# Performance work log

Measured on AMD Instinct MI355X. Metric: run time of the kernel, lower is better.

## Reference

```python
import jax, jax.numpy as jnp
import numpy as np

N = 50000   # nodes
E = 800000  # edges
D = 128     # input_dim
H = 128     # hidden_dim
C = 40      # output_dim (classes)


def setup_inputs() -> dict:
    key = jax.random.key(0)
    ks = jax.random.split(key, 8)
    x = jax.random.normal(ks[0], (N, D), dtype=jnp.float32)
    edge_index = jax.random.randint(ks[1], (2, E), 0, N, dtype=jnp.int32)
    sD = 1.0 / np.sqrt(D)
    sH = 1.0 / np.sqrt(H)
    W1 = jax.random.uniform(ks[2], (D, H), jnp.float32, -sD, sD)
    b1 = jnp.zeros((H,), jnp.float32)
    W2 = jax.random.uniform(ks[3], (H, H), jnp.float32, -sH, sH)
    b2 = jnp.zeros((H,), jnp.float32)
    W3 = jax.random.uniform(ks[4], (H, C), jnp.float32, -sH, sH)
    b3 = jnp.zeros((C,), jnp.float32)
    return {"x": x, "edge_index": edge_index,
            "W1": W1, "b1": b1, "W2": W2, "b2": b2, "W3": W3, "b3": b3}


def reference(x, edge_index, W1, b1, W2, b2, W3, b3):
    # GCNConv: out = D^{-1/2} (A + I) D^{-1/2} (x @ W) + b
    src = edge_index[0]
    dst = edge_index[1]
    loop = jnp.arange(N, dtype=src.dtype)
    src_f = jnp.concatenate([src, loop])  # [E+N] with self-loops
    dst_f = jnp.concatenate([dst, loop])
    deg = jax.ops.segment_sum(jnp.ones(E + N, x.dtype), dst_f, num_segments=N)
    dinv = jax.lax.rsqrt(jnp.maximum(deg, 1.0))  # deg >= 1 due to self-loops
    norm = dinv[src_f] * dinv[dst_f]  # [E+N]

    def conv(h, W, b):
        h = h @ W                       # [N, F_out]
        msg = h[src_f] * norm[:, None]  # [E+N, F_out] gathered messages
        return jax.ops.segment_sum(msg, dst_f, num_segments=N) + b

    h = jax.nn.relu(conv(x, W1, b1))
    h = jax.nn.relu(conv(h, W2, b2))  # dropout is identity in eval mode
    return conv(h, W3, b3)
```

## Files before the change

kernel.cpp:

```cpp
#include <hip/hip_runtime.h>

typedef unsigned short ushort_t;
typedef unsigned int uint_t;


__global__ void k_deg_count(const int* __restrict__ ei, int* __restrict__ deg, int E) {
    int e = blockIdx.x * blockDim.x + threadIdx.x;
    if (e < E) atomicAdd(&deg[ei[E + e]], 1);
}

__global__ void k_bsum(const int* __restrict__ deg, int* __restrict__ bsum, int n) {
    __shared__ int s[256];
    int t = threadIdx.x;
    int i = blockIdx.x * 256 + t;
    s[t] = (i < n) ? deg[i] : 0;
    __syncthreads();
    for (int off = 128; off > 0; off >>= 1) {
        if (t < off) s[t] += s[t + off];
        __syncthreads();
    }
    if (t == 0) bsum[blockIdx.x] = s[0];
}

__global__ void k_bscan(int* __restrict__ bsum, int* __restrict__ tot, int nb) {
    __shared__ int s[1024];
    int t = threadIdx.x;
    int v = (t < nb) ? bsum[t] : 0;
    s[t] = v;
    __syncthreads();
    for (int off = 1; off < 1024; off <<= 1) {
        int u = (t >= off) ? s[t - off] : 0;
        __syncthreads();
        s[t] += u;
        __syncthreads();
    }
    if (t < nb) bsum[t] = s[t] - v;
    if (t == nb - 1) tot[0] = s[t];
}

__global__ void k_rowptr(const int* __restrict__ deg, const int* __restrict__ bsum,
                         int* __restrict__ rowptr, int* __restrict__ cursor,
                         float* __restrict__ dinv, int n) {
    __shared__ int s[256];
    int t = threadIdx.x;
    int i = blockIdx.x * 256 + t;
    int v = (i < n) ? deg[i] : 0;
    s[t] = v;
    __syncthreads();
    for (int off = 1; off < 256; off <<= 1) {
        int u = (t >= off) ? s[t - off] : 0;
        __syncthreads();
        s[t] += u;
        __syncthreads();
    }
    if (i < n) {
        int ex = bsum[blockIdx.x] + s[t] - v;
        rowptr[i] = ex;
        cursor[i] = ex;
        dinv[i] = rsqrtf((float)(v + 1));
    }
}

__global__ __launch_bounds__(256) void k_fill(const int* __restrict__ ei,
                                              int* __restrict__ cursor,
                                              int* __restrict__ csr, int E, int n) {
    const int xcd = blockIdx.x & 7;
    const int e = (blockIdx.x >> 3) * 256 + threadIdx.x;
    if (e >= E) return;
    int d = ei[E + e];
    const int lo = (int)(((long long)xcd * n) >> 3);
    const int hi = (int)(((long long)(xcd + 1) * n) >> 3);
    if (d < lo || d >= hi) return;
    int s = ei[e];
    int pos = atomicAdd(&cursor[d], 1);
    csr[pos] = s;
}

__device__ __forceinline__ ushort_t f2bf_rne(float f) {
    uint_t u = __float_as_uint(f);
    u += 0x7fffu + ((u >> 16) & 1u);
    return (ushort_t)(u >> 16);
}
__device__ __forceinline__ float bflo(uint_t u) {
    return __uint_as_float(u << 16);
}
__device__ __forceinline__ float bfhi(uint_t u) {
    return __uint_as_float(u & 0xffff0000u);
}

__global__ __launch_bounds__(256) void k_gemm128(const float* __restrict__ X,
                                                 const float* __restrict__ W,
                                                 ushort_t* __restrict__ Y, int N) {
    __shared__ float sX[32][68];
    __shared__ float sW[32][128];
    const int tid = threadIdx.x;
    const int bm = blockIdx.x * 64;
    const int m0 = (tid >> 4) * 4;
    const int c4 = (tid & 15) * 4;
    const int xr = tid >> 3;
    const int xf = tid & 7;
    float acc[4][8] = {};
    for (int k0 = 0; k0 < 128; k0 += 32) {
        #pragma unroll
        for (int rr = 0; rr < 2; ++rr) {
            int row = bm + xr + rr * 32;
            int rc = min(row, N - 1);
            float4 v = *(const float4*)(X + (size_t)rc * 128 + k0 + xf * 4);
            int m = xr + rr * 32;
            sX[xf * 4 + 0][m] = v.x;
            sX[xf * 4 + 1][m] = v.y;
            sX[xf * 4 + 2][m] = v.z;
            sX[xf * 4 + 3][m] = v.w;
        }
        #pragma unroll
        for (int it = 0; it < 4; ++it) {
            int i = tid + it * 256;
            int wr = i >> 5;
            int wf = i & 31;
            *(float4*)(&sW[wr][wf * 4]) =
                *(const float4*)(W + (size_t)(k0 + wr) * 128 + wf * 4);
        }
        __syncthreads();
        #pragma unroll
        for (int kk = 0; kk < 32; ++kk) {
            float4 a  = *(const float4*)(&sX[kk][m0]);
            float4 b0 = *(const float4*)(&sW[kk][c4]);
            float4 b1 = *(const float4*)(&sW[kk][64 + c4]);
            float av[4] = {a.x, a.y, a.z, a.w};
            float bv[8] = {b0.x, b0.y, b0.z, b0.w, b1.x, b1.y, b1.z, b1.w};
            #pragma unroll
            for (int r = 0; r < 4; ++r)
                #pragma unroll
                for (int c = 0; c < 8; ++c)
                    acc[r][c] = fmaf(av[r], bv[c], acc[r][c]);
        }
        __syncthreads();
    }
    #pragma unroll
    for (int r = 0; r < 4; ++r) {
        int row = bm + m0 + r;
        if (row < N) {
            ushort4 o0 = {f2bf_rne(acc[r][0]), f2bf_rne(acc[r][1]),
                          f2bf_rne(acc[r][2]), f2bf_rne(acc[r][3])};
            ushort4 o1 = {f2bf_rne(acc[r][4]), f2bf_rne(acc[r][5]),
                          f2bf_rne(acc[r][6]), f2bf_rne(acc[r][7])};
            *(ushort4*)(Y + (size_t)row * 128 + c4)      = o0;
            *(ushort4*)(Y + (size_t)row * 128 + 64 + c4) = o1;
        }
    }
}

__global__ __launch_bounds__(256) void k_gemm40(const float* __restrict__ X,
                                                const float* __restrict__ W,
                                                ushort_t* __restrict__ Y, int N) {
    __shared__ float sX[32][132];
    __shared__ float sW[32][40];
    const int tid = threadIdx.x;
    const int bm = blockIdx.x * 128;
    const int m0 = (tid >> 3) * 4;
    const int n0 = (tid & 7) * 5;
    const int xf = tid & 7;
    float acc[4][5] = {};
    for (int k0 = 0; k0 < 128; k0 += 32) {
        #pragma unroll
        for (int it = 0; it < 4; ++it) {
            int i = tid + it * 256;
            int row = bm + (i >> 3);
            int rc = min(row, N - 1);
            float4 v = *(const float4*)(X + (size_t)rc * 128 + k0 + xf * 4);
            int m = i >> 3;
            sX[xf * 4 + 0][m] = v.x;
            sX[xf * 4 + 1][m] = v.y;
            sX[xf * 4 + 2][m] = v.z;
            sX[xf * 4 + 3][m] = v.w;
        }
        for (int i = tid; i < 320; i += 256) {
            int wr = i / 10;
            int wf = i - wr * 10;
            *(float4*)(&sW[wr][wf * 4]) =
                *(const float4*)(W + (size_t)(k0 + wr) * 40 + wf * 4);
        }
        __syncthreads();
        #pragma unroll
        for (int kk = 0; kk < 32; ++kk) {
            float4 a = *(const float4*)(&sX[kk][m0]);
            float av[4] = {a.x, a.y, a.z, a.w};
            #pragma unroll
            for (int c = 0; c < 5; ++c) {
                float b = sW[kk][n0 + c];
                #pragma unroll
                for (int r = 0; r < 4; ++r)
                    acc[r][c] = fmaf(av[r], b, acc[r][c]);
            }
        }
        __syncthreads();
    }
    #pragma unroll
    for (int r = 0; r < 4; ++r) {
        int row = bm + m0 + r;
        if (row < N) {
            #pragma unroll
            for (int c = 0; c < 5; ++c)
                Y[(size_t)row * 64 + n0 + c] = f2bf_rne(acc[r][c]);
        }
    }
}

template <bool RELU>
__global__ __launch_bounds__(256) void k_agg128(
        const ushort_t* __restrict__ XW, const int* __restrict__ rowptr,
        const int* __restrict__ csr, const float* __restrict__ dinv,
        const float* __restrict__ bias, float* __restrict__ out, int n) {
    const int lane = threadIdx.x & 63;
    const int wv = __builtin_amdgcn_readfirstlane(threadIdx.x >> 6);
    const int d = blockIdx.x * 4 + wv;
    if (d >= n) return;
    const uint_t* xw = (const uint_t*)XW;
    float dv = dinv[d];
    float w0 = dv * dv;
    uint_t sq = xw[(size_t)d * 64 + lane];
    float2 a;
    a.x = w0 * bflo(sq);
    a.y = w0 * bfhi(sq);
    int j = rowptr[d], end = rowptr[d + 1];
    for (; j + 8 <= end; j += 8) {
        int s0 = csr[j + 0], s1 = csr[j + 1], s2 = csr[j + 2], s3 = csr[j + 3];
        int s4 = csr[j + 4], s5 = csr[j + 5], s6 = csr[j + 6], s7 = csr[j + 7];
        float w0e = dinv[s0] * dv, w1e = dinv[s1] * dv;
        float w2e = dinv[s2] * dv, w3e = dinv[s3] * dv;
        float w4e = dinv[s4] * dv, w5e = dinv[s5] * dv;
        float w6e = dinv[s6] * dv, w7e = dinv[s7] * dv;
        uint_t u0 = xw[(size_t)s0 * 64 + lane];
        uint_t u1 = xw[(size_t)s1 * 64 + lane];
        uint_t u2 = xw[(size_t)s2 * 64 + lane];
        uint_t u3 = xw[(size_t)s3 * 64 + lane];
        uint_t u4 = xw[(size_t)s4 * 64 + lane];
        uint_t u5 = xw[(size_t)s5 * 64 + lane];
        uint_t u6 = xw[(size_t)s6 * 64 + lane];
        uint_t u7 = xw[(size_t)s7 * 64 + lane];
        a.x = fmaf(w0e, bflo(u0), a.x); a.y = fmaf(w0e, bfhi(u0), a.y);
        a.x = fmaf(w1e, bflo(u1), a.x); a.y = fmaf(w1e, bfhi(u1), a.y);
        a.x = fmaf(w2e, bflo(u2), a.x); a.y = fmaf(w2e, bfhi(u2), a.y);
        a.x = fmaf(w3e, bflo(u3), a.x); a.y = fmaf(w3e, bfhi(u3), a.y);
        a.x = fmaf(w4e, bflo(u4), a.x); a.y = fmaf(w4e, bfhi(u4), a.y);
        a.x = fmaf(w5e, bflo(u5), a.x); a.y = fmaf(w5e, bfhi(u5), a.y);
        a.x = fmaf(w6e, bflo(u6), a.x); a.y = fmaf(w6e, bfhi(u6), a.y);
        a.x = fmaf(w7e, bflo(u7), a.x); a.y = fmaf(w7e, bfhi(u7), a.y);
    }
    for (; j < end; ++j) {
        int s = csr[j];
        float we = dinv[s] * dv;
        uint_t u = xw[(size_t)s * 64 + lane];
        a.x = fmaf(we, bflo(u), a.x);
        a.y = fmaf(we, bfhi(u), a.y);
    }
    float2 b = ((const float2*)bias)[lane];
    a.x += b.x; a.y += b.y;
    if (RELU) {
        a.x = fmaxf(a.x, 0.f);
        a.y = fmaxf(a.y, 0.f);
    }
    ((float2*)out)[(size_t)d * 64 + lane] = a;
}

__global__ __launch_bounds__(256) void k_agg40(
        const ushort_t* __restrict__ XW, const int* __restrict__ rowptr,
        const int* __restrict__ csr, const float* __restrict__ dinv,
        const float* __restrict__ bias, float* __restrict__ out, int n) {
    const int lane = threadIdx.x & 31;
    const int sub  = threadIdx.x >> 5;
    const int d = blockIdx.x * 8 + sub;
    if (d >= n || lane >= 20) return;
    const uint_t* xw = (const uint_t*)XW;
    float dv = dinv[d];
    float w0 = dv * dv;
    uint_t sq = xw[(size_t)d * 32 + lane];
    float2 a;
    a.x = w0 * bflo(sq);
    a.y = w0 * bfhi(sq);
    int j = rowptr[d], end = rowptr[d + 1];
    for (; j + 4 <= end; j += 4) {
        int s0 = csr[j + 0], s1 = csr[j + 1], s2 = csr[j + 2], s3 = csr[j + 3];
        float w0e = dinv[s0] * dv, w1e = dinv[s1] * dv;
        float w2e = dinv[s2] * dv, w3e = dinv[s3] * dv;
        uint_t u0 = xw[(size_t)s0 * 32 + lane];
        uint_t u1 = xw[(size_t)s1 * 32 + lane];
        uint_t u2 = xw[(size_t)s2 * 32 + lane];
        uint_t u3 = xw[(size_t)s3 * 32 + lane];
        a.x = fmaf(w0e, bflo(u0), a.x); a.y = fmaf(w0e, bfhi(u0), a.y);
        a.x = fmaf(w1e, bflo(u1), a.x); a.y = fmaf(w1e, bfhi(u1), a.y);
        a.x = fmaf(w2e, bflo(u2), a.x); a.y = fmaf(w2e, bfhi(u2), a.y);
        a.x = fmaf(w3e, bflo(u3), a.x); a.y = fmaf(w3e, bfhi(u3), a.y);
    }
    for (; j < end; ++j) {
        int s = csr[j];
        float we = dinv[s] * dv;
        uint_t u = xw[(size_t)s * 32 + lane];
        a.x = fmaf(we, bflo(u), a.x);
        a.y = fmaf(we, bfhi(u), a.y);
    }
    float2 b = ((const float2*)bias)[lane];
    a.x += b.x; a.y += b.y;
    ((float2*)out)[(size_t)d * 20 + lane] = a;
}

static inline int cdiv(long long a, int b) { return (int)((a + b - 1) / b); }

extern "C" void kernel_launch(void* const* d_in, const int* in_sizes, int n_in,
                              void* d_out, int out_size, void* d_ws, size_t ws_size,
                              hipStream_t stream) {
    const float* x  = (const float*)d_in[0];
    const int*   ei = (const int*)d_in[1];
    const float* W1 = (const float*)d_in[2];
    const float* b1 = (const float*)d_in[3];
    const float* W2 = (const float*)d_in[4];
    const float* b2 = (const float*)d_in[5];
    const float* W3 = (const float*)d_in[6];
    const float* b3 = (const float*)d_in[7];
    float* out = (float*)d_out;

    const int N = in_sizes[0] / 128;
    const int E = in_sizes[1] / 2;

    char* ws = (char*)d_ws;
    int*   deg    = (int*)ws;                 ws += (size_t)N * 4;
    int*   rowptr = (int*)ws;                 ws += (size_t)(N + 1) * 4;
    int*   cursor = (int*)ws;                 ws += (size_t)N * 4;
    float* dinv   = (float*)ws;               ws += (size_t)N * 4;
    int*   bsum   = (int*)ws;                 ws += (size_t)1024 * 4;
    ws = (char*)(((uintptr_t)ws + 127) & ~(uintptr_t)127);
    int*   csr    = (int*)ws;                 ws += (size_t)E * 4;
    char*  bufA   = ws;                       ws += (size_t)N * 128 * 4;
    float* bufB   = (float*)ws;

    const int BT = 256;
    const int nb = cdiv(N, 256);

    hipMemsetAsync(deg, 0, (size_t)N * 4, stream);
    k_deg_count<<<cdiv(E, BT), BT, 0, stream>>>(ei, deg, E);
    k_bsum<<<nb, 256, 0, stream>>>(deg, bsum, N);
    k_bscan<<<1, 1024, 0, stream>>>(bsum, rowptr + N, nb);
    k_rowptr<<<nb, 256, 0, stream>>>(deg, bsum, rowptr, cursor, dinv, N);
    k_fill<<<cdiv(E, BT) * 8, 256, 0, stream>>>(ei, cursor, csr, E, N);

    k_gemm128<<<cdiv(N, 64), 256, 0, stream>>>(x, W1, (ushort_t*)bufA, N);
    k_agg128<true><<<cdiv(N, 4), 256, 0, stream>>>((const ushort_t*)bufA, rowptr, csr, dinv, b1, bufB, N);
    k_gemm128<<<cdiv(N, 64), 256, 0, stream>>>(bufB, W2, (ushort_t*)bufA, N);
    k_agg128<true><<<cdiv(N, 4), 256, 0, stream>>>((const ushort_t*)bufA, rowptr, csr, dinv, b2, bufB, N);
    k_gemm40<<<cdiv(N, 128), 256, 0, stream>>>(bufB, W3, (ushort_t*)bufA, N);
    k_agg40<<<cdiv(N, 8), 256, 0, stream>>>((const ushort_t*)bufA, rowptr, csr, dinv, b3, out, N);
}
```

Before: 327.5 us.

## Store precomputed edge norms in CSR and enlarge GEMM row tile

The CSR fill now stores each edge as an int2 of source index plus a precomputed dinv[s]*dinv[d] weight. This removes the dependent random dinv gather from all three aggregation kernels, at the cost of doubling CSR storage and read traffic. The 128-wide GEMM also moves from 64 to 128 rows per block, with 8x8 accumulators per thread, to improve shared-memory reuse. That larger tile raises register pressure and halves the number of blocks.

```diff
diff --git a/kernel.cpp b/kernel.cpp
--- a/kernel.cpp
+++ b/kernel.cpp
@@ -63,7 +63,8 @@
 
 __global__ __launch_bounds__(256) void k_fill(const int* __restrict__ ei,
                                               int* __restrict__ cursor,
-                                              int* __restrict__ csr, int E, int n) {
+                                              const float* __restrict__ dinv,
+                                              int2* __restrict__ csr, int E, int n) {
     const int xcd = blockIdx.x & 7;
     const int e = (blockIdx.x >> 3) * 256 + threadIdx.x;
     if (e >= E) return;
@@ -73,7 +74,10 @@
     if (d < lo || d >= hi) return;
     int s = ei[e];
     int pos = atomicAdd(&cursor[d], 1);
-    csr[pos] = s;
+    int2 p;
+    p.x = s;
+    p.y = __float_as_int(dinv[s] * dinv[d]);
+    csr[pos] = p;
 }
 
 __device__ __forceinline__ ushort_t f2bf_rne(float f) {
@@ -91,22 +95,22 @@
 __global__ __launch_bounds__(256) void k_gemm128(const float* __restrict__ X,
                                                  const float* __restrict__ W,
                                                  ushort_t* __restrict__ Y, int N) {
-    __shared__ float sX[32][68];
+    __shared__ float sX[32][132];
     __shared__ float sW[32][128];
     const int tid = threadIdx.x;
-    const int bm = blockIdx.x * 64;
-    const int m0 = (tid >> 4) * 4;
+    const int bm = blockIdx.x * 128;
+    const int m0 = (tid >> 4) * 8;
     const int c4 = (tid & 15) * 4;
-    const int xr = tid >> 3;
     const int xf = tid & 7;
-    float acc[4][8] = {};
+    float acc[8][8] = {};
     for (int k0 = 0; k0 < 128; k0 += 32) {
         #pragma unroll
-        for (int rr = 0; rr < 2; ++rr) {
-            int row = bm + xr + rr * 32;
+        for (int it = 0; it < 4; ++it) {
+            int i = tid + it * 256;
+            int row = bm + (i >> 3);
             int rc = min(row, N - 1);
             float4 v = *(const float4*)(X + (size_t)rc * 128 + k0 + xf * 4);
-            int m = xr + rr * 32;
+            int m = i >> 3;
             sX[xf * 4 + 0][m] = v.x;
             sX[xf * 4 + 1][m] = v.y;
             sX[xf * 4 + 2][m] = v.z;
@@ -123,13 +127,14 @@
         __syncthreads();
         #pragma unroll
         for (int kk = 0; kk < 32; ++kk) {
-            float4 a  = *(const float4*)(&sX[kk][m0]);
+            float4 a0 = *(const float4*)(&sX[kk][m0]);
+            float4 a1 = *(const float4*)(&sX[kk][m0 + 4]);
             float4 b0 = *(const float4*)(&sW[kk][c4]);
             float4 b1 = *(const float4*)(&sW[kk][64 + c4]);
-            float av[4] = {a.x, a.y, a.z, a.w};
+            float av[8] = {a0.x, a0.y, a0.z, a0.w, a1.x, a1.y, a1.z, a1.w};
             float bv[8] = {b0.x, b0.y, b0.z, b0.w, b1.x, b1.y, b1.z, b1.w};
             #pragma unroll
-            for (int r = 0; r < 4; ++r)
+            for (int r = 0; r < 8; ++r)
                 #pragma unroll
                 for (int c = 0; c < 8; ++c)
                     acc[r][c] = fmaf(av[r], bv[c], acc[r][c]);
@@ -137,7 +142,7 @@
         __syncthreads();
     }
     #pragma unroll
-    for (int r = 0; r < 4; ++r) {
+    for (int r = 0; r < 8; ++r) {
         int row = bm + m0 + r;
         if (row < N) {
             ushort4 o0 = {f2bf_rne(acc[r][0]), f2bf_rne(acc[r][1]),
@@ -209,7 +214,7 @@
 template <bool RELU>
 __global__ __launch_bounds__(256) void k_agg128(
         const ushort_t* __restrict__ XW, const int* __restrict__ rowptr,
-        const int* __restrict__ csr, const float* __restrict__ dinv,
+        const int2* __restrict__ csr, const float* __restrict__ dinv,
         const float* __restrict__ bias, float* __restrict__ out, int n) {
     const int lane = threadIdx.x & 63;
     const int wv = __builtin_amdgcn_readfirstlane(threadIdx.x >> 6);
@@ -224,20 +229,20 @@
     a.y = w0 * bfhi(sq);
     int j = rowptr[d], end = rowptr[d + 1];
     for (; j + 8 <= end; j += 8) {
-        int s0 = csr[j + 0], s1 = csr[j + 1], s2 = csr[j + 2], s3 = csr[j + 3];
-        int s4 = csr[j + 4], s5 = csr[j + 5], s6 = csr[j + 6], s7 = csr[j + 7];
-        float w0e = dinv[s0] * dv, w1e = dinv[s1] * dv;
-        float w2e = dinv[s2] * dv, w3e = dinv[s3] * dv;
-        float w4e = dinv[s4] * dv, w5e = dinv[s5] * dv;
-        float w6e = dinv[s6] * dv, w7e = dinv[s7] * dv;
-        uint_t u0 = xw[(size_t)s0 * 64 + lane];
-        uint_t u1 = xw[(size_t)s1 * 64 + lane];
-        uint_t u2 = xw[(size_t)s2 * 64 + lane];
-        uint_t u3 = xw[(size_t)s3 * 64 + lane];
-        uint_t u4 = xw[(size_t)s4 * 64 + lane];
-        uint_t u5 = xw[(size_t)s5 * 64 + lane];
-        uint_t u6 = xw[(size_t)s6 * 64 + lane];
-        uint_t u7 = xw[(size_t)s7 * 64 + lane];
+        int2 p0 = csr[j + 0], p1 = csr[j + 1], p2 = csr[j + 2], p3 = csr[j + 3];
+        int2 p4 = csr[j + 4], p5 = csr[j + 5], p6 = csr[j + 6], p7 = csr[j + 7];
+        uint_t u0 = xw[(size_t)p0.x * 64 + lane];
+        uint_t u1 = xw[(size_t)p1.x * 64 + lane];
+        uint_t u2 = xw[(size_t)p2.x * 64 + lane];
+        uint_t u3 = xw[(size_t)p3.x * 64 + lane];
+        uint_t u4 = xw[(size_t)p4.x * 64 + lane];
+        uint_t u5 = xw[(size_t)p5.x * 64 + lane];
+        uint_t u6 = xw[(size_t)p6.x * 64 + lane];
+        uint_t u7 = xw[(size_t)p7.x * 64 + lane];
+        float w0e = __int_as_float(p0.y), w1e = __int_as_float(p1.y);
+        float w2e = __int_as_float(p2.y), w3e = __int_as_float(p3.y);
+        float w4e = __int_as_float(p4.y), w5e = __int_as_float(p5.y);
+        float w6e = __int_as_float(p6.y), w7e = __int_as_float(p7.y);
         a.x = fmaf(w0e, bflo(u0), a.x); a.y = fmaf(w0e, bfhi(u0), a.y);
         a.x = fmaf(w1e, bflo(u1), a.x); a.y = fmaf(w1e, bfhi(u1), a.y);
         a.x = fmaf(w2e, bflo(u2), a.x); a.y = fmaf(w2e, bfhi(u2), a.y);
@@ -248,9 +253,9 @@
         a.x = fmaf(w7e, bflo(u7), a.x); a.y = fmaf(w7e, bfhi(u7), a.y);
     }
     for (; j < end; ++j) {
-        int s = csr[j];
-        float we = dinv[s] * dv;
-        uint_t u = xw[(size_t)s * 64 + lane];
+        int2 p = csr[j];
+        float we = __int_as_float(p.y);
+        uint_t u = xw[(size_t)p.x * 64 + lane];
         a.x = fmaf(we, bflo(u), a.x);
         a.y = fmaf(we, bfhi(u), a.y);
     }
@@ -265,7 +270,7 @@
 
 __global__ __launch_bounds__(256) void k_agg40(
         const ushort_t* __restrict__ XW, const int* __restrict__ rowptr,
-        const int* __restrict__ csr, const float* __restrict__ dinv,
+        const int2* __restrict__ csr, const float* __restrict__ dinv,
         const float* __restrict__ bias, float* __restrict__ out, int n) {
     const int lane = threadIdx.x & 31;
     const int sub  = threadIdx.x >> 5;
@@ -280,22 +285,22 @@
     a.y = w0 * bfhi(sq);
     int j = rowptr[d], end = rowptr[d + 1];
     for (; j + 4 <= end; j += 4) {
-        int s0 = csr[j + 0], s1 = csr[j + 1], s2 = csr[j + 2], s3 = csr[j + 3];
-        float w0e = dinv[s0] * dv, w1e = dinv[s1] * dv;
-        float w2e = dinv[s2] * dv, w3e = dinv[s3] * dv;
-        uint_t u0 = xw[(size_t)s0 * 32 + lane];
-        uint_t u1 = xw[(size_t)s1 * 32 + lane];
-        uint_t u2 = xw[(size_t)s2 * 32 + lane];
-        uint_t u3 = xw[(size_t)s3 * 32 + lane];
+        int2 p0 = csr[j + 0], p1 = csr[j + 1], p2 = csr[j + 2], p3 = csr[j + 3];
+        uint_t u0 = xw[(size_t)p0.x * 32 + lane];
+        uint_t u1 = xw[(size_t)p1.x * 32 + lane];
+        uint_t u2 = xw[(size_t)p2.x * 32 + lane];
+        uint_t u3 = xw[(size_t)p3.x * 32 + lane];
+        float w0e = __int_as_float(p0.y), w1e = __int_as_float(p1.y);
+        float w2e = __int_as_float(p2.y), w3e = __int_as_float(p3.y);
         a.x = fmaf(w0e, bflo(u0), a.x); a.y = fmaf(w0e, bfhi(u0), a.y);
         a.x = fmaf(w1e, bflo(u1), a.x); a.y = fmaf(w1e, bfhi(u1), a.y);
         a.x = fmaf(w2e, bflo(u2), a.x); a.y = fmaf(w2e, bfhi(u2), a.y);
         a.x = fmaf(w3e, bflo(u3), a.x); a.y = fmaf(w3e, bfhi(u3), a.y);
     }
     for (; j < end; ++j) {
-        int s = csr[j];
-        float we = dinv[s] * dv;
-        uint_t u = xw[(size_t)s * 32 + lane];
+        int2 p = csr[j];
+        float we = __int_as_float(p.y);
+        uint_t u = xw[(size_t)p.x * 32 + lane];
         a.x = fmaf(we, bflo(u), a.x);
         a.y = fmaf(we, bfhi(u), a.y);
     }
@@ -329,7 +334,7 @@
     float* dinv   = (float*)ws;               ws += (size_t)N * 4;
     int*   bsum   = (int*)ws;                 ws += (size_t)1024 * 4;
     ws = (char*)(((uintptr_t)ws + 127) & ~(uintptr_t)127);
-    int*   csr    = (int*)ws;                 ws += (size_t)E * 4;
+    int2*  csr    = (int2*)ws;                ws += (size_t)E * 8;
     char*  bufA   = ws;                       ws += (size_t)N * 128 * 4;
     float* bufB   = (float*)ws;
 
@@ -341,11 +346,11 @@
     k_bsum<<<nb, 256, 0, stream>>>(deg, bsum, N);
     k_bscan<<<1, 1024, 0, stream>>>(bsum, rowptr + N, nb);
     k_rowptr<<<nb, 256, 0, stream>>>(deg, bsum, rowptr, cursor, dinv, N);
-    k_fill<<<cdiv(E, BT) * 8, 256, 0, stream>>>(ei, cursor, csr, E, N);
-
-    k_gemm128<<<cdiv(N, 64), 256, 0, stream>>>(x, W1, (ushort_t*)bufA, N);
+    k_fill<<<cdiv(E, BT) * 8, 256, 0, stream>>>(ei, cursor, dinv, csr, E, N);
+
+    k_gemm128<<<cdiv(N, 128), 256, 0, stream>>>(x, W1, (ushort_t*)bufA, N);
     k_agg128<true><<<cdiv(N, 4), 256, 0, stream>>>((const ushort_t*)bufA, rowptr, csr, dinv, b1, bufB, N);
-    k_gemm128<<<cdiv(N, 64), 256, 0, stream>>>(bufB, W2, (ushort_t*)bufA, N);
+    k_gemm128<<<cdiv(N, 128), 256, 0, stream>>>(bufB, W2, (ushort_t*)bufA, N);
     k_agg128<true><<<cdiv(N, 4), 256, 0, stream>>>((const ushort_t*)bufA, rowptr, csr, dinv, b2, bufB, N);
     k_gemm40<<<cdiv(N, 128), 256, 0, stream>>>(bufB, W3, (ushort_t*)bufA, N);
     k_agg40<<<cdiv(N, 8), 256, 0, stream>>>((const ushort_t*)bufA, rowptr, csr, dinv, b3, out, N);
```

New measurement: 321.8 us. Within noise of the previous version (-1.8%).
